# Kernel tuning notes

Measured on AMD Instinct MI355X. Metric: run time of the kernel, lower is better.

Reference implementation:

```python
import jax, jax.numpy as jnp
import numpy as np

EMBED_DIM = 1024
NUM_HEADS = 16
HEAD_DIM = EMBED_DIM // NUM_HEADS


def setup_inputs() -> dict:
    key = jax.random.key(0)
    ks = jax.random.split(key, 9)
    B, S, E = 2, 2048, EMBED_DIM
    scale = 1.0 / np.sqrt(E)
    inp = {
        "x": jax.random.normal(ks[0], (B, S, E), dtype=jnp.float32),
        "Wq": jax.random.normal(ks[1], (E, E), dtype=jnp.float32) * scale,
        "bq": jnp.zeros((E,), dtype=jnp.float32),
        "Wk": jax.random.normal(ks[2], (E, E), dtype=jnp.float32) * scale,
        "bk": jnp.zeros((E,), dtype=jnp.float32),
        "Wv": jax.random.normal(ks[3], (E, E), dtype=jnp.float32) * scale,
        "bv": jnp.zeros((E,), dtype=jnp.float32),
        "Wo": jax.random.normal(ks[4], (E, E), dtype=jnp.float32) * scale,
        "bo": jnp.zeros((E,), dtype=jnp.float32),
    }
    return inp


def reference(x, Wq, bq, Wk, bk, Wv, bv, Wo, bo):
    B, S, E = x.shape
    H, D = NUM_HEADS, HEAD_DIM
    sm_scale = D ** (-0.5)

    def proj(W, b):
        # torch Linear: x @ W.T + b ; reshape to [B, H, S, D]
        y = jnp.einsum("bse,fe->bsf", x, W) + b
        return y.reshape(B, S, H, D).transpose(0, 2, 1, 3)

    q = proj(Wq, bq)  # [B, H, S, D]
    k = proj(Wk, bk)
    v = proj(Wv, bv)

    scores = jnp.einsum("bhqd,bhkd->bhqk", q, k) * sm_scale  # [B, H, S, S]
    attn = jax.nn.softmax(scores, axis=-1)
    o = jnp.einsum("bhqk,bhkd->bhqd", attn, v)  # [B, H, S, D]
    o = o.transpose(0, 2, 1, 3).reshape(B, S, E)
    return jnp.einsum("bse,fe->bsf", o, Wo) + bo
```

## Files before the change

### kernel.cpp

```cpp
#include <hip/hip_runtime.h>
#include <hip/hip_fp16.h>
#include <stdint.h>


typedef _Float16 f16;
typedef _Float16 f16x8 __attribute__((ext_vector_type(8)));
typedef _Float16 f16x4v __attribute__((ext_vector_type(4)));
typedef __fp16 hf4 __attribute__((ext_vector_type(4)));
typedef float f32x4 __attribute__((ext_vector_type(4)));

#define BQ  2
#define SEQ 2048
#define EMB 1024
#define NH  16
#define HD  64
#define MM  (BQ * SEQ)

__device__ __forceinline__ void gld_lds16(const void* g, void* l) {
  __builtin_amdgcn_global_load_lds(
      (const __attribute__((address_space(1))) void*)g,
      (__attribute__((address_space(3))) void*)l, 16, 0, 0);
}

__device__ __forceinline__ void stage128x64(const f16* __restrict__ src,
                                            int ld, f16* lds, int tid) {
#pragma unroll
  for (int it = 0; it < 4; ++it) {
    int idx = it * 256 + tid;
    int r = idx >> 3, c = idx & 7;
    int sc = c ^ (r & 7);
    gld_lds16(src + (size_t)r * ld + sc * 8, lds + idx * 8);
  }
}

__global__ void cvt4(const float* __restrict__ src, f16* __restrict__ dst,
                     int n4) {
  int i = blockIdx.x * blockDim.x + threadIdx.x;
  if (i < n4) {
    float4 v = ((const float4*)src)[i];
    f16x4v o;
    o[0] = (f16)v.x; o[1] = (f16)v.y; o[2] = (f16)v.z; o[3] = (f16)v.w;
    ((f16x4v*)dst)[i] = o;
  }
}

__global__ void cvtW4(const float* __restrict__ s0, const float* __restrict__ s1,
                      const float* __restrict__ s2, const float* __restrict__ s3,
                      f16* __restrict__ d0, f16* __restrict__ d1,
                      f16* __restrict__ d2, f16* __restrict__ d3, int n4) {
  int i = blockIdx.x * blockDim.x + threadIdx.x;
  if (i >= n4) return;
  const float* s = (blockIdx.y == 0) ? s0 : (blockIdx.y == 1) ? s1
                   : (blockIdx.y == 2) ? s2 : s3;
  f16* d = (blockIdx.y == 0) ? d0 : (blockIdx.y == 1) ? d1
           : (blockIdx.y == 2) ? d2 : d3;
  float4 v = ((const float4*)s)[i];
  f16x4v o;
  o[0] = (f16)v.x; o[1] = (f16)v.y; o[2] = (f16)v.z; o[3] = (f16)v.w;
  ((f16x4v*)d)[i] = o;
}

template <int MODE>
__global__ __launch_bounds__(256, 2) void gemm_bt(
    const f16* __restrict__ A, const f16* __restrict__ W0,
    const f16* __restrict__ W1, const f16* __restrict__ W2,
    const float* __restrict__ b0, const float* __restrict__ b1,
    const float* __restrict__ b2, f16* __restrict__ o0, f16* __restrict__ o1,
    f16* __restrict__ o2, float* __restrict__ fo) {
  __shared__ __align__(16) f16 As[128 * 64];
  __shared__ __align__(16) f16 Bs[128 * 64];

  const int tid = threadIdx.x, lane = tid & 63, wid = tid >> 6;
  const int z = blockIdx.z;
  const f16* W = (z == 0) ? W0 : (z == 1 ? W1 : W2);
  const float* bia = (z == 0) ? b0 : (z == 1 ? b1 : b2);
  f16* outp = (z == 0) ? o0 : (z == 1 ? o1 : o2);
  const int row0 = blockIdx.x * 128, col0 = blockIdx.y * 128;
  const int wr = (wid >> 1) * 64, wc = (wid & 1) * 64;
  const int rb = lane & 15, gq = lane >> 4, sw = lane & 7;

  f32x4 acc[4][4] = {};

  for (int kt = 0; kt < EMB / 64; ++kt) {
    __syncthreads();
    stage128x64(A + (size_t)row0 * EMB + kt * 64, EMB, As, tid);
    stage128x64(W + (size_t)col0 * EMB + kt * 64, EMB, Bs, tid);
    asm volatile("s_waitcnt vmcnt(0)" ::: "memory");
    __syncthreads();
#pragma unroll
    for (int kk = 0; kk < 2; ++kk) {
      f16x8 av[4], bv[4];
#pragma unroll
      for (int f = 0; f < 4; ++f) {
        av[f] = *(const f16x8*)(As + (wr + f * 16 + rb) * 64 +
                                (((kk * 4 + gq) ^ sw) << 3));
        bv[f] = *(const f16x8*)(Bs + (wc + f * 16 + rb) * 64 +
                                (((kk * 4 + gq) ^ sw) << 3));
      }
#pragma unroll
      for (int fi = 0; fi < 4; ++fi)
#pragma unroll
        for (int fj = 0; fj < 4; ++fj)
          acc[fi][fj] = __builtin_amdgcn_mfma_f32_16x16x32_f16(
              av[fi], bv[fj], acc[fi][fj], 0, 0, 0);
    }
  }

  float bias[4];
#pragma unroll
  for (int fj = 0; fj < 4; ++fj) bias[fj] = bia[col0 + wc + fj * 16 + rb];
  const float scale = (MODE == 0 && z == 0) ? 0.18033688011112042f : 1.0f;
#pragma unroll
  for (int fi = 0; fi < 4; ++fi) {
#pragma unroll
    for (int i = 0; i < 4; ++i) {
      int row = row0 + wr + fi * 16 + gq * 4 + i;
#pragma unroll
      for (int fj = 0; fj < 4; ++fj) {
        int col = col0 + wc + fj * 16 + rb;
        float v = (acc[fi][fj][i] + bias[fj]) * scale;
        if (MODE == 0) {
          int bb = row >> 11, s = row & (SEQ - 1);
          int h = col >> 6, d = col & 63;
          outp[(((size_t)(bb * NH + h)) * SEQ + s) * HD + d] = (f16)v;
        } else {
          fo[(size_t)row * EMB + col] = v;
        }
      }
    }
  }
}

__global__ __launch_bounds__(256) void vtrans(const f16* __restrict__ V,
                                              f16* __restrict__ Vt) {
  __shared__ f16 T[64][72];
  const int tid = threadIdx.x;
  const int s0 = blockIdx.x * 64, bh = blockIdx.y;
  const f16* Vh = V + (size_t)bh * SEQ * HD;
  f16* Vth = Vt + (size_t)bh * HD * SEQ;
#pragma unroll
  for (int it = 0; it < 2; ++it) {
    int idx = it * 256 + tid;
    int r = idx >> 3, c0 = (idx & 7) * 8;
    *(f16x8*)&T[r][c0] = *(const f16x8*)(Vh + (size_t)(s0 + r) * HD + c0);
  }
  __syncthreads();
#pragma unroll
  for (int it = 0; it < 2; ++it) {
    int idx = it * 256 + tid;
    int d = idx >> 3, sc = (idx & 7) * 8;
    f16x8 v;
#pragma unroll
    for (int j = 0; j < 8; ++j) v[j] = T[sc + j][d];
    *(f16x8*)(Vth + (size_t)d * SEQ + s0 + sc) = v;
  }
}

__global__ __launch_bounds__(256, 3) void attn_fwd(const f16* __restrict__ Q,
                                                   const f16* __restrict__ K,
                                                   const f16* __restrict__ Vt,
                                                   f16* __restrict__ O) {
  __shared__ __align__(16) f16 Ks[3][64 * 64];
  __shared__ __align__(16) f16 Vs[3][64 * 64];

  const int tid = threadIdx.x, lane = tid & 63, wid = tid >> 6;
  const int orig = blockIdx.x;
  const int swz = ((orig & 7) << 6) + (orig >> 3);
  const int qt = swz & 15, bh = swz >> 4;
  const f16* Qh = Q + (size_t)bh * SEQ * HD;
  const f16* Kh = K + (size_t)bh * SEQ * HD;
  const f16* Vth = Vt + (size_t)bh * HD * SEQ;
  const int q0 = qt * 128 + wid * 32;
  const int rb = lane & 15, gq = lane >> 4, sw = lane & 7;

  f16x8 aq[2][2];
#pragma unroll
  for (int qf = 0; qf < 2; ++qf)
#pragma unroll
    for (int kk = 0; kk < 2; ++kk)
      aq[qf][kk] = *(const f16x8*)(Qh + (size_t)(q0 + qf * 16 + rb) * HD +
                                   kk * 32 + gq * 8);
  asm volatile("s_waitcnt vmcnt(0)" ::: "memory");

  const int srow = tid >> 3, scol = (tid & 7) ^ (srow & 7);
  const f16* Kg0 = Kh + (size_t)srow * HD + scol * 8;
  const f16* Vg0 = Vth + (size_t)srow * SEQ + scol * 8;

  const int NT = SEQ / 64;
#pragma unroll
  for (int p = 0; p < 2; ++p) {
    const f16* kg = Kg0 + (size_t)p * 64 * HD;
    const f16* vg = Vg0 + p * 64;
    gld_lds16(kg,            &Ks[p][tid * 8]);
    gld_lds16(kg + 32 * HD,  &Ks[p][(tid + 256) * 8]);
    gld_lds16(vg,            &Vs[p][tid * 8]);
    gld_lds16(vg + 32 * SEQ, &Vs[p][(tid + 256) * 8]);
  }

  int voffb[4];
#pragma unroll
  for (int cf = 0; cf < 4; ++cf)
    voffb[cf] = rb * 64 + (((2 * cf + (gq >> 1)) ^ sw) << 3) + ((gq & 1) << 2);

  hf4 onesv;
#pragma unroll
  for (int j = 0; j < 4; ++j) onesv[j] = (__fp16)1.0f;

  f32x4 oacc[2][4] = {};
  f32x4 lacc[2] = {};

  for (int t = 0; t < NT; ++t) {
    __builtin_amdgcn_s_barrier();
    __builtin_amdgcn_sched_barrier(0);
    {
      const int tp = (t + 2 < NT) ? t + 2 : NT - 1;
      f16* Kn = &Ks[(t + 2) % 3][0];
      f16* Vn = &Vs[(t + 2) % 3][0];
      const f16* kg = Kg0 + (size_t)tp * 64 * HD;
      const f16* vg = Vg0 + tp * 64;
      gld_lds16(kg,            Kn + tid * 8);
      gld_lds16(kg + 32 * HD,  Kn + (tid + 256) * 8);
      gld_lds16(vg,            Vn + tid * 8);
      gld_lds16(vg + 32 * SEQ, Vn + (tid + 256) * 8);
      asm volatile("s_waitcnt vmcnt(8)" ::: "memory");
    }
    __builtin_amdgcn_s_barrier();
    __builtin_amdgcn_sched_barrier(0);

    const f16* Kb = &Ks[t % 3][0];
    const f16* Vb = &Vs[t % 3][0];

    f32x4 s_[2][4] = {};
#pragma unroll
    for (int kk = 0; kk < 2; ++kk) {
      f16x8 bk[4];
#pragma unroll
      for (int cf = 0; cf < 4; ++cf)
        bk[cf] = *(const f16x8*)(Kb + (cf * 16 + rb) * 64 +
                                 (((kk * 4 + gq) ^ sw) << 3));
#pragma unroll
      for (int qf = 0; qf < 2; ++qf)
#pragma unroll
        for (int cf = 0; cf < 4; ++cf)
          s_[qf][cf] = __builtin_amdgcn_mfma_f32_16x16x32_f16(
              bk[cf], aq[qf][kk], s_[qf][cf], 0, 0, 0);
    }

    hf4 pa[2][4];
#pragma unroll
    for (int qf = 0; qf < 2; ++qf)
#pragma unroll
      for (int cf = 0; cf < 4; ++cf) {
        float e0 = __builtin_amdgcn_exp2f(s_[qf][cf][0]);
        float e1 = __builtin_amdgcn_exp2f(s_[qf][cf][1]);
        float e2 = __builtin_amdgcn_exp2f(s_[qf][cf][2]);
        float e3 = __builtin_amdgcn_exp2f(s_[qf][cf][3]);
        auto h01 = __builtin_amdgcn_cvt_pkrtz(e0, e1);
        auto h23 = __builtin_amdgcn_cvt_pkrtz(e2, e3);
        hf4 w;
        w[0] = h01[0]; w[1] = h01[1]; w[2] = h23[0]; w[3] = h23[1];
        pa[qf][cf] = w;
      }

#pragma unroll
    for (int cf = 0; cf < 4; ++cf) {
      hf4 vb[4];
#pragma unroll
      for (int df = 0; df < 4; ++df)
        vb[df] = *(const hf4*)(Vb + voffb[cf] + df * 1024);
#pragma unroll
      for (int qf = 0; qf < 2; ++qf) {
        lacc[qf] = __builtin_amdgcn_mfma_f32_16x16x16f16(pa[qf][cf], onesv,
                                                         lacc[qf], 0, 0, 0);
#pragma unroll
        for (int df = 0; df < 4; ++df)
          oacc[qf][df] = __builtin_amdgcn_mfma_f32_16x16x16f16(
              pa[qf][cf], vb[df], oacc[qf][df], 0, 0, 0);
      }
    }
  }
  asm volatile("s_waitcnt vmcnt(0)" ::: "memory");

  const int b = bh >> 4, h = bh & 15;
#pragma unroll
  for (int qf = 0; qf < 2; ++qf)
#pragma unroll
    for (int i = 0; i < 4; ++i) {
      const float inv = 1.0f / lacc[qf][i];
      const int s = q0 + qf * 16 + gq * 4 + i;
      f16* orow = O + ((size_t)(b * SEQ + s)) * EMB + h * 64 + rb;
#pragma unroll
      for (int df = 0; df < 4; ++df)
        orow[df * 16] = (f16)(oacc[qf][df][i] * inv);
    }
}

extern "C" void kernel_launch(void* const* d_in, const int* in_sizes, int n_in,
                              void* d_out, int out_size, void* d_ws,
                              size_t ws_size, hipStream_t stream) {
  const float* x = (const float*)d_in[0];
  const float* Wq = (const float*)d_in[1];
  const float* bq = (const float*)d_in[2];
  const float* Wk = (const float*)d_in[3];
  const float* bk = (const float*)d_in[4];
  const float* Wv = (const float*)d_in[5];
  const float* bv = (const float*)d_in[6];
  const float* Wo = (const float*)d_in[7];
  const float* bo = (const float*)d_in[8];
  float* out = (float*)d_out;

  const size_t NX = (size_t)MM * EMB;
  const size_t NW = (size_t)EMB * EMB;

  f16* xh  = (f16*)d_ws;
  f16* wqh = xh + NX;
  f16* wkh = wqh + NW;
  f16* wvh = wkh + NW;
  f16* woh = wvh + NW;
  f16* Qw  = woh + NW;
  f16* Kw  = Qw + NX;
  f16* Vw  = Kw + NX;
  f16* Vtw = Vw + NX;
  f16* Ow  = Vtw + NX;

  cvt4<<<(int)(NX / 4 / 256), 256, 0, stream>>>(x, xh, (int)(NX / 4));
  cvtW4<<<dim3((int)(NW / 4 / 256), 4), 256, 0, stream>>>(
      Wq, Wk, Wv, Wo, wqh, wkh, wvh, woh, (int)(NW / 4));

  gemm_bt<0><<<dim3(MM / 128, EMB / 128, 3), 256, 0, stream>>>(
      xh, wqh, wkh, wvh, bq, bk, bv, Qw, Kw, Vw, nullptr);

  vtrans<<<dim3(SEQ / 64, BQ * NH), 256, 0, stream>>>(Vw, Vtw);

  attn_fwd<<<dim3(512), 256, 0, stream>>>(Qw, Kw, Vtw, Ow);

  gemm_bt<1><<<dim3(MM / 128, EMB / 128, 1), 256, 0, stream>>>(
      Ow, woh, woh, woh, bo, bo, bo, nullptr, nullptr, nullptr, out);
}
```

Before: 114.4 us.

## Use 16x16x32 MFMA for PV and compute row sums with VALU instead of MFMA

Switches the P·V product from 16x16x16 to 16x16x32 f16 MFMA, packing eight exponentials per operand, and changes the V-transpose store layout so each lane can read eight contiguous V values with one LDS load. The softmax denominator is now summed in registers and reduced with cross-lane shuffles at the end, replacing the extra MFMA against a ones vector. This halves the PV MFMA instruction count and removes the denominator MFMAs, at the cost of VALU adds and a permuted Vt layout that must stay consistent with the loads.

```diff
diff --git a/kernel.cpp b/kernel.cpp
--- a/kernel.cpp
+++ b/kernel.cpp
@@ -6,8 +6,8 @@
 typedef _Float16 f16;
 typedef _Float16 f16x8 __attribute__((ext_vector_type(8)));
 typedef _Float16 f16x4v __attribute__((ext_vector_type(4)));
-typedef __fp16 hf4 __attribute__((ext_vector_type(4)));
 typedef float f32x4 __attribute__((ext_vector_type(4)));
+typedef int i32x4 __attribute__((ext_vector_type(4)));
 
 #define BQ  2
 #define SEQ 2048
@@ -31,6 +31,16 @@
     int sc = c ^ (r & 7);
     gld_lds16(src + (size_t)r * ld + sc * 8, lds + idx * 8);
   }
+}
+
+__device__ __forceinline__ f16x8 pack8(float a0, float a1, float a2, float a3,
+                                       float b0, float b1, float b2, float b3) {
+  i32x4 w;
+  w.x = __builtin_bit_cast(int, __builtin_amdgcn_cvt_pkrtz(a0, a1));
+  w.y = __builtin_bit_cast(int, __builtin_amdgcn_cvt_pkrtz(a2, a3));
+  w.z = __builtin_bit_cast(int, __builtin_amdgcn_cvt_pkrtz(b0, b1));
+  w.w = __builtin_bit_cast(int, __builtin_amdgcn_cvt_pkrtz(b2, b3));
+  return __builtin_bit_cast(f16x8, w);
 }
 
 __global__ void cvt4(const float* __restrict__ src, f16* __restrict__ dst,
@@ -148,11 +158,17 @@
 #pragma unroll
   for (int it = 0; it < 2; ++it) {
     int idx = it * 256 + tid;
-    int d = idx >> 3, sc = (idx & 7) * 8;
+    int d = idx >> 3, a = idx & 7;
     f16x8 v;
 #pragma unroll
-    for (int j = 0; j < 8; ++j) v[j] = T[sc + j][d];
-    *(f16x8*)(Vth + (size_t)d * SEQ + s0 + sc) = v;
+    for (int j = 0; j < 8; ++j) v[j] = T[a * 8 + j][d];
+    const int base = ((a >> 2) << 5) + ((a & 1) << 4) + (((a >> 1) & 1) << 2);
+    f16* dst = Vth + (size_t)d * SEQ + s0 + base;
+    f16x4v w0, w1;
+#pragma unroll
+    for (int j = 0; j < 4; ++j) { w0[j] = v[j]; w1[j] = v[4 + j]; }
+    *(f16x4v*)dst = w0;
+    *(f16x4v*)(dst + 8) = w1;
   }
 }
 
@@ -163,7 +179,8 @@
   __shared__ __align__(16) f16 Ks[3][64 * 64];
   __shared__ __align__(16) f16 Vs[3][64 * 64];
 
-  const int tid = threadIdx.x, lane = tid & 63, wid = tid >> 6;
+  const int tid = threadIdx.x, lane = tid & 63;
+  const int wid = tid >> 6;
   const int orig = blockIdx.x;
   const int swz = ((orig & 7) << 6) + (orig >> 3);
   const int qt = swz & 15, bh = swz >> 4;
@@ -197,17 +214,8 @@
     gld_lds16(vg + 32 * SEQ, &Vs[p][(tid + 256) * 8]);
   }
 
-  int voffb[4];
-#pragma unroll
-  for (int cf = 0; cf < 4; ++cf)
-    voffb[cf] = rb * 64 + (((2 * cf + (gq >> 1)) ^ sw) << 3) + ((gq & 1) << 2);
-
-  hf4 onesv;
-#pragma unroll
-  for (int j = 0; j < 4; ++j) onesv[j] = (__fp16)1.0f;
-
   f32x4 oacc[2][4] = {};
-  f32x4 lacc[2] = {};
+  float lsum[2] = {0.f, 0.f};
 
   for (int t = 0; t < NT; ++t) {
     __builtin_amdgcn_s_barrier();
@@ -246,47 +254,55 @@
               bk[cf], aq[qf][kk], s_[qf][cf], 0, 0, 0);
     }
 
-    hf4 pa[2][4];
+    f16x8 bp[2][2];
 #pragma unroll
     for (int qf = 0; qf < 2; ++qf)
 #pragma unroll
-      for (int cf = 0; cf < 4; ++cf) {
-        float e0 = __builtin_amdgcn_exp2f(s_[qf][cf][0]);
-        float e1 = __builtin_amdgcn_exp2f(s_[qf][cf][1]);
-        float e2 = __builtin_amdgcn_exp2f(s_[qf][cf][2]);
-        float e3 = __builtin_amdgcn_exp2f(s_[qf][cf][3]);
-        auto h01 = __builtin_amdgcn_cvt_pkrtz(e0, e1);
-        auto h23 = __builtin_amdgcn_cvt_pkrtz(e2, e3);
-        hf4 w;
-        w[0] = h01[0]; w[1] = h01[1]; w[2] = h23[0]; w[3] = h23[1];
-        pa[qf][cf] = w;
+      for (int g = 0; g < 2; ++g) {
+        float e0 = __builtin_amdgcn_exp2f(s_[qf][2 * g][0]);
+        float e1 = __builtin_amdgcn_exp2f(s_[qf][2 * g][1]);
+        float e2 = __builtin_amdgcn_exp2f(s_[qf][2 * g][2]);
+        float e3 = __builtin_amdgcn_exp2f(s_[qf][2 * g][3]);
+        float f0 = __builtin_amdgcn_exp2f(s_[qf][2 * g + 1][0]);
+        float f1 = __builtin_amdgcn_exp2f(s_[qf][2 * g + 1][1]);
+        float f2 = __builtin_amdgcn_exp2f(s_[qf][2 * g + 1][2]);
+        float f3 = __builtin_amdgcn_exp2f(s_[qf][2 * g + 1][3]);
+        lsum[qf] += ((e0 + e1) + (e2 + e3)) + ((f0 + f1) + (f2 + f3));
+        bp[qf][g] = pack8(e0, e1, e2, e3, f0, f1, f2, f3);
       }
 
 #pragma unroll
-    for (int cf = 0; cf < 4; ++cf) {
-      hf4 vb[4];
-#pragma unroll
-      for (int df = 0; df < 4; ++df)
-        vb[df] = *(const hf4*)(Vb + voffb[cf] + df * 1024);
-#pragma unroll
-      for (int qf = 0; qf < 2; ++qf) {
-        lacc[qf] = __builtin_amdgcn_mfma_f32_16x16x16f16(pa[qf][cf], onesv,
-                                                         lacc[qf], 0, 0, 0);
-#pragma unroll
-        for (int df = 0; df < 4; ++df)
-          oacc[qf][df] = __builtin_amdgcn_mfma_f32_16x16x16f16(
-              pa[qf][cf], vb[df], oacc[qf][df], 0, 0, 0);
+    for (int g = 0; g < 2; ++g) {
+#pragma unroll
+      for (int df = 0; df < 4; ++df) {
+        f16x8 vb = *(const f16x8*)(Vb + (df * 16 + rb) * 64 +
+                                   (((g * 4 + gq) ^ sw) << 3));
+        oacc[0][df] = __builtin_amdgcn_mfma_f32_16x16x32_f16(bp[0][g], vb,
+                                                             oacc[0][df], 0, 0, 0);
+        oacc[1][df] = __builtin_amdgcn_mfma_f32_16x16x32_f16(bp[1][g], vb,
+                                                             oacc[1][df], 0, 0, 0);
       }
     }
   }
   asm volatile("s_waitcnt vmcnt(0)" ::: "memory");
 
+  float lv[2];
+#pragma unroll
+  for (int qf = 0; qf < 2; ++qf) {
+    float l = lsum[qf];
+    l += __shfl_xor(l, 16, 64);
+    l += __shfl_xor(l, 32, 64);
+    lv[qf] = l;
+  }
+
   const int b = bh >> 4, h = bh & 15;
 #pragma unroll
   for (int qf = 0; qf < 2; ++qf)
 #pragma unroll
     for (int i = 0; i < 4; ++i) {
-      const float inv = 1.0f / lacc[qf][i];
+      const int rsel = (gq * 4 + i) & 15;
+      const float l = __shfl(lv[qf], (lane & 48) + rsel, 64);
+      const float inv = 1.0f / l;
       const int s = q0 + qf * 16 + gq * 4 + i;
       f16* orow = O + ((size_t)(b * SEQ + s)) * EMB + h * 64 + rb;
 #pragma unroll
```

Result: faster. 109.2 us (-4.6%).
